# Optimization experiments

Measured on AMD Instinct MI355X. Metric: run time of the kernel, lower is better.

The kernel has to match this reference:

```python
import jax, jax.numpy as jnp
import numpy as np

N_NODES = 50000
N_EDGES = 800000
N_GRAPHS = 1024
IN_DIM, HID, OUT_DIM = 78, 256, 128
EPS = 1e-5


def setup_inputs() -> dict:
    key = jax.random.key(0)
    ks = jax.random.split(key, 12)
    def lin(k, fi, fo):
        s = 1.0 / np.sqrt(fi)
        return jax.random.uniform(k, (fi, fo), jnp.float32, -s, s)
    inp = {
        "x_l": jax.random.normal(ks[0], (N_NODES, IN_DIM), jnp.float32),
        "edge_index_l": jax.random.randint(ks[1], (2, N_EDGES), 0, N_NODES, jnp.int64),
        "batch_l": jnp.sort(jax.random.randint(ks[2], (N_NODES,), 0, N_GRAPHS, jnp.int64)),
        # GraphConv 1: 78 -> 256 (lin_rel has bias, lin_root no bias)
        "W1_rel": lin(ks[3], IN_DIM, HID), "b1_rel": jnp.zeros((HID,), jnp.float32), "W1_root": lin(ks[4], IN_DIM, HID),
        # GraphConv 2: 256 -> 512
        "W2_rel": lin(ks[5], HID, 2 * HID), "b2_rel": jnp.zeros((2 * HID,), jnp.float32), "W2_root": lin(ks[6], HID, 2 * HID),
        # GraphConv 3: 512 -> 512
        "W3_rel": lin(ks[7], 2 * HID, 2 * HID), "b3_rel": jnp.zeros((2 * HID,), jnp.float32), "W3_root": lin(ks[8], 2 * HID, 2 * HID),
        # fc1: Linear(512 -> 128) + LayerNorm(128); Dropout(0.01) is identity in eval
        "W_fc": lin(ks[9], 2 * HID, OUT_DIM), "b_fc": jnp.zeros((OUT_DIM,), jnp.float32),
        "ln_g": jnp.ones((OUT_DIM,), jnp.float32), "ln_b": jnp.zeros((OUT_DIM,), jnp.float32),
    }
    return inp


def _graph_conv(x, src, dst, W_rel, b_rel, W_root):
    # PyG GraphConv (aggr='add'): out = lin_rel(sum_{j->i} x_j) + lin_root(x_i)
    aggr = jax.ops.segment_sum(x[src], dst, num_segments=x.shape[0])  # [N, d_in]
    return aggr @ W_rel + b_rel + x @ W_root


def reference(x_l, edge_index_l, batch_l,
              W1_rel, b1_rel, W1_root,
              W2_rel, b2_rel, W2_root,
              W3_rel, b3_rel, W3_root,
              W_fc, b_fc, ln_g, ln_b):
    src, dst = edge_index_l[0], edge_index_l[1]
    h = jax.nn.relu(_graph_conv(x_l, src, dst, W1_rel, b1_rel, W1_root))
    h = jax.nn.relu(_graph_conv(h, src, dst, W2_rel, b2_rel, W2_root))
    h = jax.nn.relu(_graph_conv(h, src, dst, W3_rel, b3_rel, W3_root))
    # fc1: Linear -> LayerNorm -> Dropout(0.01, identity in eval) -> ReLU
    z = h @ W_fc + b_fc
    mu = jnp.mean(z, axis=-1, keepdims=True)
    var = jnp.mean(jnp.square(z - mu), axis=-1, keepdims=True)
    z = (z - mu) * jax.lax.rsqrt(var + EPS) * ln_g + ln_b
    x_atom = jax.nn.relu(z)  # [N, OUT_DIM]
    pooled = jax.ops.segment_sum(x_atom, batch_l, num_segments=N_GRAPHS)  # [G, OUT_DIM]
    return (x_atom, pooled)
```

## Files before the change

### kernel.cpp

```cpp
#include <hip/hip_runtime.h>

#define N_NODES 50000
#define N_EDGES 800000
#define N_GRAPHS 1024
#define IN_DIM 78
#define K1P 96
#define HID 256
#define OUT_DIM 128

typedef unsigned short ushort_t;
typedef __attribute__((ext_vector_type(8))) short v8s;
typedef __attribute__((ext_vector_type(4))) float v4f;
typedef __attribute__((ext_vector_type(2))) unsigned short us2;
typedef __attribute__((ext_vector_type(4))) unsigned short us4;
typedef __attribute__((ext_vector_type(8))) unsigned short us8;

__device__ __forceinline__ ushort_t f2bf(float f) {
    unsigned u = __float_as_uint(f);
    unsigned r = (u + 0x7fffu + ((u >> 16) & 1u)) >> 16;
    return (ushort_t)r;
}
__device__ __forceinline__ float bf2f(ushort_t h) {
    return __uint_as_float((unsigned)h << 16);
}

#define GLOAD_LDS16(g, l) \
    __builtin_amdgcn_global_load_lds( \
        (const __attribute__((address_space(1))) unsigned int*)(g), \
        (__attribute__((address_space(3))) unsigned int*)(l), 16, 0, 0)

__global__ __launch_bounds__(256)
void wt_kernel(const float* __restrict__ W, ushort_t* __restrict__ out,
               int K, int N, int Kp)
{
    int i = blockIdx.x * 256 + threadIdx.x;
    if (i >= N * Kp) return;
    int n = i / Kp, k = i - n * Kp;
    float v = (k < K) ? W[(size_t)k * N + n] : 0.0f;
    out[i] = f2bf(v);
}

__global__ __launch_bounds__(256)
void pad_cast_kernel(const float* __restrict__ in, ushort_t* __restrict__ out,
                     int rows, int Kin, int Kout)
{
    int i = blockIdx.x * 256 + threadIdx.x;
    if (i >= rows * Kout) return;
    int r = i / Kout, k = i - r * Kout;
    out[i] = f2bf(k < Kin ? in[(size_t)r * Kin + k] : 0.0f);
}

__global__ __launch_bounds__(256)
void hist_kernel(const int* __restrict__ dstI, int* __restrict__ deg, int nE)
{
    int e = blockIdx.x * 256 + threadIdx.x;
    if (e < nE) {
        int d = dstI[e];
        if ((unsigned)d < (unsigned)N_NODES) atomicAdd(&deg[d], 1);
    }
}

__global__ __launch_bounds__(1024)
void scan1_kernel(const int* __restrict__ deg, int* __restrict__ rowptr,
                  int* __restrict__ blocksum, int n)
{
    __shared__ int s[1024];
    int b = (int)blockIdx.x, t = (int)threadIdx.x;
    int i = b * 1024 + t;
    int v = (i < n) ? deg[i] : 0;
    s[t] = v;
    __syncthreads();
    for (int off = 1; off < 1024; off <<= 1) {
        int a = (t >= off) ? s[t - off] : 0;
        __syncthreads();
        s[t] += a;
        __syncthreads();
    }
    if (i < n) rowptr[i + 1] = s[t];
    if (t == 1023) blocksum[b] = s[1023];
    if (b == 0 && t == 0) rowptr[0] = 0;
}

__global__ __launch_bounds__(64)
void scan2_kernel(int* __restrict__ blocksum, int nb)
{
    int t = (int)threadIdx.x;
    int v = (t < nb) ? blocksum[t] : 0;
    #pragma unroll
    for (int off = 1; off < 64; off <<= 1) {
        int a = __shfl_up(v, off, 64);
        if (t >= off) v += a;
    }
    if (t < nb) blocksum[t] = v;
}

__global__ __launch_bounds__(256)
void scan3_kernel(const int* __restrict__ blocksum, int* __restrict__ rowptr,
                  int* __restrict__ cursor, int n)
{
    int j = blockIdx.x * 256 + threadIdx.x;
    if (j > n) return;
    int v;
    if (j == 0) v = 0;
    else {
        int b = (j - 1) >> 10;
        v = rowptr[j] + (b >= 1 ? blocksum[b - 1] : 0);
    }
    rowptr[j] = v;
    if (j < n) cursor[j] = v;
}

__global__ __launch_bounds__(256)
void fill_kernel(const int* __restrict__ srcI, const int* __restrict__ dstI,
                 int* __restrict__ cursor, int* __restrict__ csr_src, int nE)
{
    int e = blockIdx.x * 256 + threadIdx.x;
    if (e < nE) {
        int d = dstI[e];
        int s = srcI[e];
        if ((unsigned)d < (unsigned)N_NODES && (unsigned)s < (unsigned)N_NODES) {
            int pos = atomicAdd(&cursor[d], 1);
            csr_src[pos] = s;
        }
    }
}

template<int VPT> struct VecT;
template<> struct VecT<2> { using T = us2; };
template<> struct VecT<4> { using T = us4; };
template<> struct VecT<8> { using T = us8; };

template<int VPT>
__global__ __launch_bounds__(256)
void csr_agg_wave_kernel(const ushort_t* __restrict__ feat,
                         const int* __restrict__ rowptr,
                         const int* __restrict__ csr_src,
                         ushort_t* __restrict__ out, int Ds)
{
    using T = typename VecT<VPT>::T;
    const int wv   = (int)threadIdx.x >> 6;
    const int node = (int)blockIdx.x * 4 + wv;
    if (node >= N_NODES) return;
    const int lane = (int)threadIdx.x & 63;
    const int off0 = lane * VPT;
    const bool act = off0 < Ds;
    const int off  = act ? off0 : (Ds - VPT);

    const int e0 = rowptr[node], e1 = rowptr[node + 1];
    float acc[VPT];
    #pragma unroll
    for (int i = 0; i < VPT; ++i) acc[i] = 0.0f;

    int e = e0;
    for (; e + 4 <= e1; e += 4) {
        int s0 = csr_src[e + 0];
        int s1 = csr_src[e + 1];
        int s2 = csr_src[e + 2];
        int s3 = csr_src[e + 3];
        T r0 = *(const T*)(feat + (size_t)s0 * Ds + off);
        T r1 = *(const T*)(feat + (size_t)s1 * Ds + off);
        T r2 = *(const T*)(feat + (size_t)s2 * Ds + off);
        T r3 = *(const T*)(feat + (size_t)s3 * Ds + off);
        #pragma unroll
        for (int i = 0; i < VPT; ++i)
            acc[i] += (bf2f(r0[i]) + bf2f(r1[i])) + (bf2f(r2[i]) + bf2f(r3[i]));
    }
    for (; e < e1; ++e) {
        int s = csr_src[e];
        T r = *(const T*)(feat + (size_t)s * Ds + off);
        #pragma unroll
        for (int i = 0; i < VPT; ++i) acc[i] += bf2f(r[i]);
    }

    if (act) {
        T o;
        #pragma unroll
        for (int i = 0; i < VPT; ++i) o[i] = f2bf(acc[i]);
        *(T*)(out + (size_t)node * Ds + off0) = o;
    }
}

template<int NT>
__global__ __launch_bounds__(256, 2)
void mfma_gemm_kernel(const ushort_t* __restrict__ A1,
                      const ushort_t* __restrict__ A2,
                      const ushort_t* __restrict__ W1t,
                      const ushort_t* __restrict__ W2t,
                      const float* __restrict__ bias,
                      void* __restrict__ outp,
                      int M, int K, int Fo, int relu, int out_bf16)
{
    constexpr int BN      = NT * 32;
    constexpr int NBT     = NT * 2;
    constexpr int BT_PW   = NBT / 4;
    __shared__ ushort_t Al[8 * 512];
    __shared__ ushort_t Bl[NBT * 512];
    const int tid = (int)threadIdx.x;
    const int l   = tid & 63;
    const int w   = tid >> 6;
    const int q   = l >> 4;
    const int r15 = l & 15;
    const int bm  = blockIdx.y * 128;
    const int bn  = blockIdx.x * BN;
    const int wm  = w >> 1, wn = w & 1;

    v4f acc[4][NT];
    #pragma unroll
    for (int mt = 0; mt < 4; ++mt)
        #pragma unroll
        for (int nt = 0; nt < NT; ++nt)
            acc[mt][nt] = (v4f){0.0f, 0.0f, 0.0f, 0.0f};

    for (int pass = 0; pass < 2; ++pass) {
        const ushort_t* A  = pass ? A2  : A1;
        const ushort_t* Bt = pass ? W2t : W1t;
        if (A == nullptr) break;
        for (int k0 = 0; k0 < K; k0 += 32) {
            __syncthreads();
            #pragma unroll
            for (int ii = 0; ii < 2; ++ii) {
                int it = w * 2 + ii;
                int row = bm + it * 16 + r15;
                const ushort_t* ga = A + (size_t)row * K + k0 + q * 8;
                if (row < M) GLOAD_LDS16(ga, Al + it * 512);
            }
            #pragma unroll
            for (int jj = 0; jj < BT_PW; ++jj) {
                int jt = w * BT_PW + jj;
                int col = bn + jt * 16 + r15;
                const ushort_t* gb = Bt + (size_t)col * K + k0 + q * 8;
                GLOAD_LDS16(gb, Bl + jt * 512);
            }
            __syncthreads();
            v8s af[4], bf[NT];
            #pragma unroll
            for (int mt = 0; mt < 4; ++mt)
                af[mt] = *(const v8s*)(Al + (wm * 4 + mt) * 512 + l * 8);
            #pragma unroll
            for (int nt = 0; nt < NT; ++nt)
                bf[nt] = *(const v8s*)(Bl + (wn * NT + nt) * 512 + l * 8);
            #pragma unroll
            for (int mt = 0; mt < 4; ++mt)
                #pragma unroll
                for (int nt = 0; nt < NT; ++nt)
                    acc[mt][nt] = __builtin_amdgcn_mfma_f32_16x16x32_bf16(
                        af[mt], bf[nt], acc[mt][nt], 0, 0, 0);
        }
    }

    #pragma unroll
    for (int nt = 0; nt < NT; ++nt) {
        int col = bn + wn * (NT * 16) + nt * 16 + r15;
        float bb = bias[col];
        #pragma unroll
        for (int mt = 0; mt < 4; ++mt) {
            #pragma unroll
            for (int p = 0; p < 4; ++p) {
                int row = bm + wm * 64 + mt * 16 + q * 4 + p;
                if (row < M) {
                    float v = acc[mt][nt][p] + bb;
                    if (relu) v = fmaxf(v, 0.0f);
                    if (out_bf16) ((ushort_t*)outp)[(size_t)row * Fo + col] = f2bf(v);
                    else          ((float*)outp)[(size_t)row * Fo + col]   = v;
                }
            }
        }
    }
}

__global__ __launch_bounds__(128)
void ln_relu_pool_kernel(const float* __restrict__ z,
                         const float* __restrict__ gamma,
                         const float* __restrict__ beta,
                         const int* __restrict__ batch,
                         float* __restrict__ x_atom,
                         float* __restrict__ pooled)
{
    int row = (int)blockIdx.x;
    int t = (int)threadIdx.x;
    float v = z[(long long)row * 128 + t];

    __shared__ float red[2];
    float s = v;
    #pragma unroll
    for (int o = 32; o >= 1; o >>= 1) s += __shfl_xor(s, o, 64);
    int wave = t >> 6;
    if ((t & 63) == 0) red[wave] = s;
    __syncthreads();
    float mean = (red[0] + red[1]) * (1.0f / 128.0f);

    float d = v - mean;
    float s2 = d * d;
    #pragma unroll
    for (int o = 32; o >= 1; o >>= 1) s2 += __shfl_xor(s2, o, 64);
    __syncthreads();
    if ((t & 63) == 0) red[wave] = s2;
    __syncthreads();
    float var = (red[0] + red[1]) * (1.0f / 128.0f);

    float y = d * rsqrtf(var + 1e-5f) * gamma[t] + beta[t];
    y = fmaxf(y, 0.0f);
    x_atom[(long long)row * 128 + t] = y;
    int b = batch[row];
    if ((unsigned)b < (unsigned)N_GRAPHS)
        atomicAdd(pooled + (long long)b * 128 + t, y);
}

extern "C" void kernel_launch(void* const* d_in, const int* in_sizes, int n_in,
                              void* d_out, int out_size, void* d_ws, size_t ws_size,
                              hipStream_t stream)
{
    const float* x     = (const float*)d_in[0];
    const int*   ei    = (const int*)d_in[1];
    const int*   batch = (const int*)d_in[2];
    const float* W1r   = (const float*)d_in[3];
    const float* b1    = (const float*)d_in[4];
    const float* W1o   = (const float*)d_in[5];
    const float* W2r   = (const float*)d_in[6];
    const float* b2    = (const float*)d_in[7];
    const float* W2o   = (const float*)d_in[8];
    const float* W3r   = (const float*)d_in[9];
    const float* b3    = (const float*)d_in[10];
    const float* W3o   = (const float*)d_in[11];
    const float* Wfc   = (const float*)d_in[12];
    const float* bfc   = (const float*)d_in[13];
    const float* lng   = (const float*)d_in[14];
    const float* lnb   = (const float*)d_in[15];

    const size_t WS_NEED = 204800000;
    if (ws_size < WS_NEED) {
        hipMemsetAsync(d_out, 0, (size_t)out_size * sizeof(float), stream);
        return;
    }

    char* ws = (char*)d_ws;
    ushort_t* xb   = (ushort_t*)(ws + 0);
    ushort_t* h1   = (ushort_t*)(ws + 9600000);
    float*    z    = (float*)   (ws + 0);
    ushort_t* aggr = (ushort_t*)(ws + 35200000);
    ushort_t* h2   = (ushort_t*)(ws + 86400000);
    ushort_t* h3   = (ushort_t*)(ws + 137600000);
    int* deg    = (int*)(ws + 188800000);
    int* rowptr = (int*)(ws + 189000000);
    int* cursor = (int*)(ws + 189200128);
    int* csrsrc = (int*)(ws + 189400128);
    int* blksum = (int*)(ws + 192600128);
    ushort_t* wt = (ushort_t*)(ws + 192600512);
    ushort_t* w1r_t = wt;
    ushort_t* w1o_t = w1r_t + 24576;
    ushort_t* w2r_t = w1o_t + 24576;
    ushort_t* w2o_t = w2r_t + 131072;
    ushort_t* w3r_t = w2o_t + 131072;
    ushort_t* w3o_t = w3r_t + 262144;
    ushort_t* wfc_t = w3o_t + 262144;

    float* x_atom = (float*)d_out;
    float* pooled = x_atom + (size_t)N_NODES * OUT_DIM;

    const int* src = ei;
    const int* dst = ei + N_EDGES;

    wt_kernel<<<(256 * K1P + 255) / 256, 256, 0, stream>>>(W1r, w1r_t, IN_DIM, HID, K1P);
    wt_kernel<<<(256 * K1P + 255) / 256, 256, 0, stream>>>(W1o, w1o_t, IN_DIM, HID, K1P);
    wt_kernel<<<(512 * 256 + 255) / 256, 256, 0, stream>>>(W2r, w2r_t, HID, 2 * HID, HID);
    wt_kernel<<<(512 * 256 + 255) / 256, 256, 0, stream>>>(W2o, w2o_t, HID, 2 * HID, HID);
    wt_kernel<<<(512 * 512 + 255) / 256, 256, 0, stream>>>(W3r, w3r_t, 2 * HID, 2 * HID, 2 * HID);
    wt_kernel<<<(512 * 512 + 255) / 256, 256, 0, stream>>>(W3o, w3o_t, 2 * HID, 2 * HID, 2 * HID);
    wt_kernel<<<(128 * 512 + 255) / 256, 256, 0, stream>>>(Wfc, wfc_t, 2 * HID, OUT_DIM, 2 * HID);
    pad_cast_kernel<<<((N_NODES * K1P) + 255) / 256, 256, 0, stream>>>(x, xb, N_NODES, IN_DIM, K1P);

    hipMemsetAsync(deg, 0, N_NODES * sizeof(int), stream);
    hist_kernel<<<(N_EDGES + 255) / 256, 256, 0, stream>>>(dst, deg, N_EDGES);
    {
        int nb = (N_NODES + 1023) / 1024;
        scan1_kernel<<<nb, 1024, 0, stream>>>(deg, rowptr, blksum, N_NODES);
        scan2_kernel<<<1, 64, 0, stream>>>(blksum, nb);
        scan3_kernel<<<(N_NODES + 1 + 255) / 256, 256, 0, stream>>>(blksum, rowptr, cursor, N_NODES);
    }
    fill_kernel<<<(N_EDGES + 255) / 256, 256, 0, stream>>>(src, dst, cursor, csrsrc, N_EDGES);

    const int GY = (N_NODES + 127) / 128;
    const int AGG_BLKS = (N_NODES + 3) / 4;

    csr_agg_wave_kernel<2><<<AGG_BLKS, 256, 0, stream>>>(xb, rowptr, csrsrc, aggr, K1P);
    {
        dim3 g(HID / 256, GY);
        mfma_gemm_kernel<8><<<g, 256, 0, stream>>>(aggr, xb, w1r_t, w1o_t, b1, h1,
                                                   N_NODES, K1P, HID, 1, 1);
    }
    csr_agg_wave_kernel<4><<<AGG_BLKS, 256, 0, stream>>>(h1, rowptr, csrsrc, aggr, HID);
    {
        dim3 g((2 * HID) / 256, GY);
        mfma_gemm_kernel<8><<<g, 256, 0, stream>>>(aggr, h1, w2r_t, w2o_t, b2, h2,
                                                   N_NODES, HID, 2 * HID, 1, 1);
    }
    csr_agg_wave_kernel<8><<<AGG_BLKS, 256, 0, stream>>>(h2, rowptr, csrsrc, aggr, 2 * HID);
    {
        dim3 g((2 * HID) / 256, GY);
        mfma_gemm_kernel<8><<<g, 256, 0, stream>>>(aggr, h2, w3r_t, w3o_t, b3, h3,
                                                   N_NODES, 2 * HID, 2 * HID, 1, 1);
    }
    {
        dim3 g(OUT_DIM / 128, GY);
        mfma_gemm_kernel<4><<<g, 256, 0, stream>>>(h3, nullptr, wfc_t, nullptr, bfc, z,
                                                   N_NODES, 2 * HID, OUT_DIM, 0, 0);
    }
    hipMemsetAsync(pooled, 0, (size_t)N_GRAPHS * OUT_DIM * sizeof(float), stream);
    ln_relu_pool_kernel<<<N_NODES, 128, 0, stream>>>(z, lng, lnb, batch, x_atom, pooled);
}
```

Baseline: 718.1 us.

## Register-prefetch next K-step in MFMA GEMM instead of direct global-to-LDS loads

The GEMM main loop now loads the next K tile from global memory into registers while the current tile is consumed from LDS, then writes the registers to LDS at the start of the next step. This replaces the synchronous global_load_lds path, which stalled on every step, with software pipelining across the two passes flattened into a single step loop. It costs extra VGPRs and an explicit LDS write per step, which could hurt occupancy under the launch bounds of 2 blocks per CU.

Result: no change. 717.9 us (-0.0%).

```diff
diff --git a/kernel.cpp b/kernel.cpp
--- a/kernel.cpp
+++ b/kernel.cpp
@@ -11,6 +11,7 @@
 typedef unsigned short ushort_t;
 typedef __attribute__((ext_vector_type(8))) short v8s;
 typedef __attribute__((ext_vector_type(4))) float v4f;
+typedef __attribute__((ext_vector_type(4))) unsigned int u4;
 typedef __attribute__((ext_vector_type(2))) unsigned short us2;
 typedef __attribute__((ext_vector_type(4))) unsigned short us4;
 typedef __attribute__((ext_vector_type(8))) unsigned short us8;
@@ -23,11 +24,6 @@
 __device__ __forceinline__ float bf2f(ushort_t h) {
     return __uint_as_float((unsigned)h << 16);
 }
-
-#define GLOAD_LDS16(g, l) \
-    __builtin_amdgcn_global_load_lds( \
-        (const __attribute__((address_space(1))) unsigned int*)(g), \
-        (__attribute__((address_space(3))) unsigned int*)(l), 16, 0, 0)
 
 __global__ __launch_bounds__(256)
 void wt_kernel(const float* __restrict__ W, ushort_t* __restrict__ out,
@@ -190,11 +186,11 @@
                       void* __restrict__ outp,
                       int M, int K, int Fo, int relu, int out_bf16)
 {
-    constexpr int BN      = NT * 32;
-    constexpr int NBT     = NT * 2;
-    constexpr int BT_PW   = NBT / 4;
-    __shared__ ushort_t Al[8 * 512];
-    __shared__ ushort_t Bl[NBT * 512];
+    constexpr int BN    = NT * 32;
+    constexpr int NBT   = NT * 2;
+    constexpr int BT_PW = NBT / 4;
+    __shared__ __align__(16) ushort_t Al[8 * 512];
+    __shared__ __align__(16) ushort_t Bl[NBT * 512];
     const int tid = (int)threadIdx.x;
     const int l   = tid & 63;
     const int w   = tid >> 6;
@@ -204,6 +200,9 @@
     const int bn  = blockIdx.x * BN;
     const int wm  = w >> 1, wn = w & 1;
 
+    const int s1 = K >> 5;
+    const int nsteps = A2 ? (2 * s1) : s1;
+
     v4f acc[4][NT];
     #pragma unroll
     for (int mt = 0; mt < 4; ++mt)
@@ -211,41 +210,50 @@
         for (int nt = 0; nt < NT; ++nt)
             acc[mt][nt] = (v4f){0.0f, 0.0f, 0.0f, 0.0f};
 
-    for (int pass = 0; pass < 2; ++pass) {
-        const ushort_t* A  = pass ? A2  : A1;
-        const ushort_t* Bt = pass ? W2t : W1t;
-        if (A == nullptr) break;
-        for (int k0 = 0; k0 < K; k0 += 32) {
-            __syncthreads();
-            #pragma unroll
-            for (int ii = 0; ii < 2; ++ii) {
-                int it = w * 2 + ii;
-                int row = bm + it * 16 + r15;
-                const ushort_t* ga = A + (size_t)row * K + k0 + q * 8;
-                if (row < M) GLOAD_LDS16(ga, Al + it * 512);
-            }
-            #pragma unroll
-            for (int jj = 0; jj < BT_PW; ++jj) {
-                int jt = w * BT_PW + jj;
-                int col = bn + jt * 16 + r15;
-                const ushort_t* gb = Bt + (size_t)col * K + k0 + q * 8;
-                GLOAD_LDS16(gb, Bl + jt * 512);
-            }
-            __syncthreads();
-            v8s af[4], bf[NT];
-            #pragma unroll
-            for (int mt = 0; mt < 4; ++mt)
-                af[mt] = *(const v8s*)(Al + (wm * 4 + mt) * 512 + l * 8);
+    u4 ra[2], rb[BT_PW];
+    auto load_step = [&](int step) {
+        const ushort_t* A  = (step >= s1) ? A2  : A1;
+        const ushort_t* Bt = (step >= s1) ? W2t : W1t;
+        const int k0 = ((step >= s1) ? (step - s1) : step) << 5;
+        #pragma unroll
+        for (int ii = 0; ii < 2; ++ii) {
+            int it  = w * 2 + ii;
+            int row = bm + it * 16 + r15;
+            if (row < M) ra[ii] = *(const u4*)(A + (size_t)row * K + k0 + q * 8);
+            else         ra[ii] = (u4){0u, 0u, 0u, 0u};
+        }
+        #pragma unroll
+        for (int jj = 0; jj < BT_PW; ++jj) {
+            int jt  = w * BT_PW + jj;
+            int col = bn + jt * 16 + r15;
+            rb[jj] = *(const u4*)(Bt + (size_t)col * K + k0 + q * 8);
+        }
+    };
+
+    load_step(0);
+    for (int step = 0; step < nsteps; ++step) {
+        __syncthreads();
+        #pragma unroll
+        for (int ii = 0; ii < 2; ++ii)
+            *(u4*)(Al + (size_t)(w * 2 + ii) * 512 + l * 8) = ra[ii];
+        #pragma unroll
+        for (int jj = 0; jj < BT_PW; ++jj)
+            *(u4*)(Bl + (size_t)(w * BT_PW + jj) * 512 + l * 8) = rb[jj];
+        if (step + 1 < nsteps) load_step(step + 1);
+        __syncthreads();
+        v8s af[4], bf[NT];
+        #pragma unroll
+        for (int mt = 0; mt < 4; ++mt)
+            af[mt] = *(const v8s*)(Al + (size_t)(wm * 4 + mt) * 512 + l * 8);
+        #pragma unroll
+        for (int nt = 0; nt < NT; ++nt)
+            bf[nt] = *(const v8s*)(Bl + (size_t)(wn * NT + nt) * 512 + l * 8);
+        #pragma unroll
+        for (int mt = 0; mt < 4; ++mt)
             #pragma unroll
             for (int nt = 0; nt < NT; ++nt)
-                bf[nt] = *(const v8s*)(Bl + (wn * NT + nt) * 512 + l * 8);
-            #pragma unroll
-            for (int mt = 0; mt < 4; ++mt)
-                #pragma unroll
-                for (int nt = 0; nt < NT; ++nt)
-                    acc[mt][nt] = __builtin_amdgcn_mfma_f32_16x16x32_bf16(
-                        af[mt], bf[nt], acc[mt][nt], 0, 0, 0);
-        }
+                acc[mt][nt] = __builtin_amdgcn_mfma_f32_16x16x32_bf16(
+                    af[mt], bf[nt], acc[mt][nt], 0, 0, 0);
     }
 
     #pragma unroll
```

## Load GEMM MFMA operands directly from global memory, dropping LDS staging

Applied to the files above, without the earlier changes.

The GEMM kernel no longer stages A and B tiles through shared memory with global_load_lds and two barriers per k-step. Each wave now loads its MFMA fragments straight from global memory through precomputed row and column pointers, and the k loop is unrolled. Output tiles shrink from 256 to 128 columns and launch bounds allow 3 blocks per SM, giving more blocks and higher occupancy. In exchange, operands are no longer shared between waves in a block, so global and L2 traffic rises and the loads become uncoalesced, strided 16-byte accesses.

After: 868.0 us. 20.9% more time.

```diff
diff --git a/kernel.cpp b/kernel.cpp
--- a/kernel.cpp
+++ b/kernel.cpp
@@ -23,11 +23,6 @@
 __device__ __forceinline__ float bf2f(ushort_t h) {
     return __uint_as_float((unsigned)h << 16);
 }
-
-#define GLOAD_LDS16(g, l) \
-    __builtin_amdgcn_global_load_lds( \
-        (const __attribute__((address_space(1))) unsigned int*)(g), \
-        (__attribute__((address_space(3))) unsigned int*)(l), 16, 0, 0)
 
 __global__ __launch_bounds__(256)
 void wt_kernel(const float* __restrict__ W, ushort_t* __restrict__ out,
@@ -181,8 +176,8 @@
 }
 
 template<int NT>
-__global__ __launch_bounds__(256, 2)
-void mfma_gemm_kernel(const ushort_t* __restrict__ A1,
+__global__ __launch_bounds__(256, 3)
+void mfma_gemm_direct(const ushort_t* __restrict__ A1,
                       const ushort_t* __restrict__ A2,
                       const ushort_t* __restrict__ W1t,
                       const ushort_t* __restrict__ W2t,
@@ -190,18 +185,13 @@
                       void* __restrict__ outp,
                       int M, int K, int Fo, int relu, int out_bf16)
 {
-    constexpr int BN      = NT * 32;
-    constexpr int NBT     = NT * 2;
-    constexpr int BT_PW   = NBT / 4;
-    __shared__ ushort_t Al[8 * 512];
-    __shared__ ushort_t Bl[NBT * 512];
     const int tid = (int)threadIdx.x;
     const int l   = tid & 63;
     const int w   = tid >> 6;
     const int q   = l >> 4;
     const int r15 = l & 15;
     const int bm  = blockIdx.y * 128;
-    const int bn  = blockIdx.x * BN;
+    const int bn  = blockIdx.x * (NT * 32);
     const int wm  = w >> 1, wn = w & 1;
 
     v4f acc[4][NT];
@@ -211,34 +201,39 @@
         for (int nt = 0; nt < NT; ++nt)
             acc[mt][nt] = (v4f){0.0f, 0.0f, 0.0f, 0.0f};
 
+    int arow[4], bcol[NT];
+    #pragma unroll
+    for (int mt = 0; mt < 4; ++mt) {
+        int row = bm + wm * 64 + mt * 16 + r15;
+        arow[mt] = (row < M) ? row : (M - 1);
+    }
+    #pragma unroll
+    for (int nt = 0; nt < NT; ++nt)
+        bcol[nt] = bn + wn * (NT * 16) + nt * 16 + r15;
+
+    const int nks = K >> 5;
     for (int pass = 0; pass < 2; ++pass) {
         const ushort_t* A  = pass ? A2  : A1;
         const ushort_t* Bt = pass ? W2t : W1t;
         if (A == nullptr) break;
-        for (int k0 = 0; k0 < K; k0 += 32) {
-            __syncthreads();
-            #pragma unroll
-            for (int ii = 0; ii < 2; ++ii) {
-                int it = w * 2 + ii;
-                int row = bm + it * 16 + r15;
-                const ushort_t* ga = A + (size_t)row * K + k0 + q * 8;
-                if (row < M) GLOAD_LDS16(ga, Al + it * 512);
-            }
-            #pragma unroll
-            for (int jj = 0; jj < BT_PW; ++jj) {
-                int jt = w * BT_PW + jj;
-                int col = bn + jt * 16 + r15;
-                const ushort_t* gb = Bt + (size_t)col * K + k0 + q * 8;
-                GLOAD_LDS16(gb, Bl + jt * 512);
-            }
-            __syncthreads();
+        const ushort_t* ap[4];
+        const ushort_t* bp[NT];
+        #pragma unroll
+        for (int mt = 0; mt < 4; ++mt)
+            ap[mt] = A + (size_t)arow[mt] * K + q * 8;
+        #pragma unroll
+        for (int nt = 0; nt < NT; ++nt)
+            bp[nt] = Bt + (size_t)bcol[nt] * K + q * 8;
+
+        #pragma unroll 4
+        for (int ks = 0; ks < nks; ++ks) {
             v8s af[4], bf[NT];
             #pragma unroll
             for (int mt = 0; mt < 4; ++mt)
-                af[mt] = *(const v8s*)(Al + (wm * 4 + mt) * 512 + l * 8);
+                af[mt] = *(const v8s*)(ap[mt] + ks * 32);
             #pragma unroll
             for (int nt = 0; nt < NT; ++nt)
-                bf[nt] = *(const v8s*)(Bl + (wn * NT + nt) * 512 + l * 8);
+                bf[nt] = *(const v8s*)(bp[nt] + ks * 32);
             #pragma unroll
             for (int mt = 0; mt < 4; ++mt)
                 #pragma unroll
@@ -250,7 +245,7 @@
 
     #pragma unroll
     for (int nt = 0; nt < NT; ++nt) {
-        int col = bn + wn * (NT * 16) + nt * 16 + r15;
+        int col = bcol[nt];
         float bb = bias[col];
         #pragma unroll
         for (int mt = 0; mt < 4; ++mt) {
@@ -384,25 +379,25 @@
 
     csr_agg_wave_kernel<2><<<AGG_BLKS, 256, 0, stream>>>(xb, rowptr, csrsrc, aggr, K1P);
     {
-        dim3 g(HID / 256, GY);
-        mfma_gemm_kernel<8><<<g, 256, 0, stream>>>(aggr, xb, w1r_t, w1o_t, b1, h1,
+        dim3 g(HID / 128, GY);
+        mfma_gemm_direct<4><<<g, 256, 0, stream>>>(aggr, xb, w1r_t, w1o_t, b1, h1,
                                                    N_NODES, K1P, HID, 1, 1);
     }
     csr_agg_wave_kernel<4><<<AGG_BLKS, 256, 0, stream>>>(h1, rowptr, csrsrc, aggr, HID);
     {
-        dim3 g((2 * HID) / 256, GY);
-        mfma_gemm_kernel<8><<<g, 256, 0, stream>>>(aggr, h1, w2r_t, w2o_t, b2, h2,
+        dim3 g((2 * HID) / 128, GY);
+        mfma_gemm_direct<4><<<g, 256, 0, stream>>>(aggr, h1, w2r_t, w2o_t, b2, h2,
                                                    N_NODES, HID, 2 * HID, 1, 1);
     }
     csr_agg_wave_kernel<8><<<AGG_BLKS, 256, 0, stream>>>(h2, rowptr, csrsrc, aggr, 2 * HID);
     {
-        dim3 g((2 * HID) / 256, GY);
-        mfma_gemm_kernel<8><<<g, 256, 0, stream>>>(aggr, h2, w3r_t, w3o_t, b3, h3,
+        dim3 g((2 * HID) / 128, GY);
+        mfma_gemm_direct<4><<<g, 256, 0, stream>>>(aggr, h2, w3r_t, w3o_t, b3, h3,
                                                    N_NODES, 2 * HID, 2 * HID, 1, 1);
     }
     {
         dim3 g(OUT_DIM / 128, GY);
-        mfma_gemm_kernel<4><<<g, 256, 0, stream>>>(h3, nullptr, wfc_t, nullptr, bfc, z,
+        mfma_gemm_direct<4><<<g, 256, 0, stream>>>(h3, nullptr, wfc_t, nullptr, bfc, z,
                                                    N_NODES, 2 * HID, OUT_DIM, 0, 0);
     }
     hipMemsetAsync(pooled, 0, (size_t)N_GRAPHS * OUT_DIM * sizeof(float), stream);
```
